# Performance work log

Measured on AMD Instinct MI355X. Metric: run time of the kernel, lower is better.

## Reference

```python
import jax, jax.numpy as jnp
import numpy as np

N_USERS, N_ITEMS, D, B = 16384, 4096, 64, 2048
NAN_FRAC = 0.7
EPS = 1e-8


def setup_inputs() -> dict:
    key = jax.random.key(0)
    k1, k2, k3, k4, k5 = jax.random.split(key, 5)
    ratings = jax.random.uniform(k1, (N_USERS, N_ITEMS), jnp.float32, 1.0, 5.0)
    miss = jax.random.uniform(k2, (N_USERS, N_ITEMS)) < NAN_FRAC
    rating_matrix = jnp.where(miss, jnp.nan, ratings)
    user_embeddings = jax.random.normal(k3, (N_USERS, D), jnp.float32)
    user_indices = jax.random.randint(k4, (B,), 0, N_USERS)
    item_indices = jax.random.randint(k5, (B,), 0, N_ITEMS)
    return {
        "rating_matrix": rating_matrix,
        "user_embeddings": user_embeddings,
        "user_indices": user_indices,
        "item_indices": item_indices,
    }


def reference(rating_matrix, user_embeddings, user_indices, item_indices):
    n_users = rating_matrix.shape[0]

    # per-user average over non-NaN ratings (0.0 if user has no ratings)
    valid_r = ~jnp.isnan(rating_matrix)                      # [N, I]
    r0 = jnp.where(valid_r, rating_matrix, 0.0)
    cnt = valid_r.sum(axis=1)
    avg_ratings = jnp.where(cnt > 0, r0.sum(axis=1) / jnp.maximum(cnt, 1), 0.0)  # [N]

    u = user_embeddings[user_indices]                        # [B, d]
    # cosine similarity of each query user vs all users
    dots = jnp.einsum('bd,nd->bn', u, user_embeddings)       # [B, N]
    mag_u = jnp.linalg.norm(u, axis=1, keepdims=True)        # [B, 1]
    mag_v = jnp.linalg.norm(user_embeddings, axis=1)[None]   # [1, N]
    sim = dots / (mag_u * mag_v + EPS)                       # [B, N]

    # ratings of all users on each query item
    ratings_col = rating_matrix[:, item_indices].T           # [B, N]
    mask = ~jnp.isnan(ratings_col)                           # valid neighbor ratings
    mask = mask & (jnp.arange(n_users)[None, :] != user_indices[:, None])  # exclude self

    diff = jnp.where(mask, ratings_col - avg_ratings[None, :], 0.0)
    sim_m = jnp.where(mask, sim, 0.0)
    num = (diff * sim_m).sum(axis=1)                         # [B]
    den = jnp.abs(sim_m).sum(axis=1)                         # [B]
    den_safe = jnp.where(den == 0, 1.0, den)

    avg_u = avg_ratings[user_indices]
    return jnp.where(den == 0, avg_u, avg_u + num / den_safe)
```

## Files before the change

kernel.cpp:

```cpp
#include <hip/hip_runtime.h>
#include <math.h>

#define NU   16384
#define NI   4096
#define DDIM 64
#define BB   2048

typedef unsigned short u16;
typedef unsigned char  u8;
typedef __attribute__((ext_vector_type(8))) short short8;
typedef __attribute__((ext_vector_type(4))) float f32x4;

static __device__ __forceinline__ u16 f2bf(float f) {
    union { float f; unsigned int u; } v; v.f = f;
    unsigned int u = v.u + 0x7FFFu + ((v.u >> 16) & 1u);
    return (u16)(u >> 16);
}

static __device__ __forceinline__ u8 enc_r(float r) {
    return (u8)__float2uint_rz(fmaf(r, 50.f, -48.5f));
}

__global__ __launch_bounds__(256) void k_qprep(
    const float* __restrict__ E, const int* __restrict__ uidx,
    u16* __restrict__ Ubf, int2* __restrict__ qinfo)
{
    const int lane = threadIdx.x & 63;
    const int b = blockIdx.x * 4 + (threadIdx.x >> 6);
    const int ub = uidx[b];
    const float e = E[(size_t)ub * DDIM + lane];
    float ss = e * e;
#pragma unroll
    for (int o = 32; o > 0; o >>= 1) ss += __shfl_xor(ss, o);
    Ubf[b * DDIM + lane] = f2bf(e);
    if (lane == 0) qinfo[b] = make_int2(ub, __float_as_int(rsqrtf(ss)));
}

__global__ __launch_bounds__(256, 8) void k_stream(
    const float* __restrict__ R, const float* __restrict__ E,
    const int* __restrict__ iidx,
    float2* __restrict__ avgInv, u8* __restrict__ Gq)
{
    __shared__ u16 s_ii[BB];
    __shared__ u8  wrow[4][NI];
    const int tid  = threadIdx.x;
    const int lane = tid & 63;
    const int wid  = tid >> 6;

    for (int t = tid; t < BB; t += 256) s_ii[t] = (u16)iidx[t];
    __syncthreads();

    const int wg = blockIdx.x * 4 + wid;
#pragma unroll 1
    for (int rr = 0; rr < 2; ++rr) {
        const int n = wg * 2 + rr;
        const float4* R4 = (const float4*)(R + (size_t)n * NI);
        const float e = E[(size_t)n * DDIM + lane];

        float sum = 0.f;
        unsigned cnti = 0;
#pragma unroll 1
        for (int h = 0; h < 2; ++h) {
            float4 v[8];
#pragma unroll
            for (int j = 0; j < 8; ++j) v[j] = R4[(h * 8 + j) * 64 + lane];
#pragma unroll
            for (int j = 0; j < 8; ++j) {
                const float4 x = v[j];
                sum += (x.x == x.x ? x.x : 0.f);
                sum += (x.y == x.y ? x.y : 0.f);
                sum += (x.z == x.z ? x.z : 0.f);
                sum += (x.w == x.w ? x.w : 0.f);
                cnti += (unsigned)__popcll(__ballot(x.x == x.x));
                cnti += (unsigned)__popcll(__ballot(x.y == x.y));
                cnti += (unsigned)__popcll(__ballot(x.z == x.z));
                cnti += (unsigned)__popcll(__ballot(x.w == x.w));
                uchar4 q;
                q.x = enc_r(x.x); q.y = enc_r(x.y); q.z = enc_r(x.z); q.w = enc_r(x.w);
                *(uchar4*)&wrow[wid][((h * 8 + j) * 64 + lane) * 4] = q;
            }
        }
        float ss = e * e;
#pragma unroll
        for (int o = 32; o > 0; o >>= 1) {
            ss  += __shfl_xor(ss, o);
            sum += __shfl_xor(sum, o);
        }
        if (lane == 0) {
            const float C = (float)cnti;
            avgInv[n] = make_float2((C > 0.f) ? (sum / C) : 0.f, rsqrtf(ss));
        }
        asm volatile("s_waitcnt lgkmcnt(0)" ::: "memory");

        u8* Gn = Gq + (size_t)n * BB;
#pragma unroll
        for (int t = 0; t < 8; ++t) {
            const int b4 = (t * 64 + lane) * 4;
            const ushort4 ii = *(const ushort4*)&s_ii[b4];
            uchar4 q;
            q.x = wrow[wid][ii.x];
            q.y = wrow[wid][ii.y];
            q.z = wrow[wid][ii.z];
            q.w = wrow[wid][ii.w];
            *(uchar4*)&Gn[b4] = q;
        }
    }
}

__global__ __launch_bounds__(256) void k_accum(
    const float* __restrict__ E, const u16* __restrict__ Ubf,
    const u8* __restrict__ Gq, const float2* __restrict__ avgInv,
    const int2* __restrict__ qinfo, float2* __restrict__ partials)
{
    const int tid  = threadIdx.x;
    const int lane = tid & 63;
    const int wid  = tid >> 6;
    const int lo   = lane & 15;
    const int hi   = lane >> 4;
    const int n0   = blockIdx.x * 16;

    short8 a[2];
#pragma unroll
    for (int kg = 0; kg < 2; ++kg) {
        const float* ep = E + (size_t)(n0 + lo) * DDIM + kg * 32 + hi * 8;
        const float4 e0 = *(const float4*)(ep);
        const float4 e1 = *(const float4*)(ep + 4);
        union { short8 v; u16 u[8]; } t;
        t.u[0] = f2bf(e0.x); t.u[1] = f2bf(e0.y); t.u[2] = f2bf(e0.z); t.u[3] = f2bf(e0.w);
        t.u[4] = f2bf(e1.x); t.u[5] = f2bf(e1.y); t.u[6] = f2bf(e1.z); t.u[7] = f2bf(e1.w);
        a[kg] = t.v;
    }
    float avr[4], ivr[4];
#pragma unroll
    for (int r = 0; r < 4; ++r) {
        const float2 ai = avgInv[n0 + hi * 4 + r];
        avr[r] = ai.x; ivr[r] = ai.y;
    }

    float2* pout = partials + (size_t)blockIdx.x * BB;

#pragma unroll 1
    for (int j = 0; j < 32; ++j) {
        const int b0 = (j * 4 + wid) * 16;
        const int2 q = qinfo[b0 + lo];
        const float inv_mu = __int_as_float(q.y);

        const short8 bf0 = *(const short8*)(Ubf + (size_t)(b0 + lo) * DDIM + hi * 8);
        const short8 bf1 = *(const short8*)(Ubf + (size_t)(b0 + lo) * DDIM + 32 + hi * 8);

        f32x4 c = {0.f, 0.f, 0.f, 0.f};
        c = __builtin_amdgcn_mfma_f32_16x16x32_bf16(a[0], bf0, c, 0, 0, 0);
        c = __builtin_amdgcn_mfma_f32_16x16x32_bf16(a[1], bf1, c, 0, 0, 0);

        float fnum = 0.f, fden = 0.f;
#pragma unroll
        for (int r = 0; r < 4; ++r) {
            const int nr = n0 + hi * 4 + r;
            const u8 qg = Gq[(size_t)nr * BB + b0 + lo];
            const bool valid = (qg != 0) && (nr != q.x);
            const float gv = (float)(int)qg * 0.02f + 0.98f;
            const float s  = valid ? c[r] * (inv_mu * ivr[r]) : 0.f;
            fnum += (gv - avr[r]) * s;
            fden += fabsf(s);
        }
        fnum += __shfl_xor(fnum, 16); fden += __shfl_xor(fden, 16);
        fnum += __shfl_xor(fnum, 32); fden += __shfl_xor(fden, 32);
        if (lane < 16) pout[b0 + lane] = make_float2(fnum, fden);
    }
}

__global__ __launch_bounds__(256) void k_final(
    const float2* __restrict__ partials, const int2* __restrict__ qinfo,
    const float2* __restrict__ avgInv, float* __restrict__ out)
{
    __shared__ float sn[8][32], sd[8][32];
    const int tid = threadIdx.x;
    const int bl  = tid & 31;
    const int ch  = tid >> 5;
    const int b   = blockIdx.x * 32 + bl;
    float n = 0.f, d = 0.f;
    for (int blk = ch; blk < NU / 16; blk += 8) {
        const float2 p = partials[(size_t)blk * BB + b];
        n += p.x; d += p.y;
    }
    sn[ch][bl] = n; sd[ch][bl] = d;
    __syncthreads();
    if (tid < 32) {
        float N = 0.f, D = 0.f;
#pragma unroll
        for (int c2 = 0; c2 < 8; ++c2) { N += sn[c2][tid]; D += sd[c2][tid]; }
        const int bb = blockIdx.x * 32 + tid;
        const float au = avgInv[qinfo[bb].x].x;
        out[bb] = (D == 0.f) ? au : (au + N / D);
    }
}

extern "C" void kernel_launch(void* const* d_in, const int* in_sizes, int n_in,
                              void* d_out, int out_size, void* d_ws, size_t ws_size,
                              hipStream_t stream)
{
    const float* R    = (const float*)d_in[0];
    const float* E    = (const float*)d_in[1];
    const int*   uidx = (const int*)d_in[2];
    const int*   iidx = (const int*)d_in[3];
    float* out = (float*)d_out;

    char* p = (char*)d_ws;
    float2* parts  = (float2*)p;  p += (size_t)(NU / 16) * BB * 8;
    u8*     Gq     = (u8*)p;      p += (size_t)NU * BB;
    u16*    Ubf    = (u16*)p;     p += (size_t)BB * DDIM * 2;
    int2*   qinfo  = (int2*)p;    p += (size_t)BB * 8;
    float2* avgInv = (float2*)p;  p += (size_t)NU * 8;

    k_qprep<<<BB / 4, 256, 0, stream>>>(E, uidx, Ubf, qinfo);
    k_stream<<<NU / 8, 256, 0, stream>>>(R, E, iidx, avgInv, Gq);
    k_accum<<<NU / 16, 256, 0, stream>>>(E, Ubf, Gq, avgInv, qinfo, parts);
    k_final<<<BB / 32, 256, 0, stream>>>(parts, qinfo, avgInv, out);
}
```

Baseline: 444.2 us.

## Software-pipeline rating row loads in k_stream with double-buffered LDS rows

k_stream now unrolls its two rows per wave by hand and issues the global loads for the second rating row while the first row is being processed. This overlaps HBM latency with compute. Each wave gets two LDS row buffers, and the per-row count moves from ballot/popcount to a float counter reduced by shuffles. The cost is a doubled LDS footprint, more registers (launch bounds lowered from 8 to 4 blocks per CU), and therefore lower occupancy.

```diff
diff --git a/kernel.cpp b/kernel.cpp
--- a/kernel.cpp
+++ b/kernel.cpp
@@ -36,13 +36,13 @@
     if (lane == 0) qinfo[b] = make_int2(ub, __float_as_int(rsqrtf(ss)));
 }
 
-__global__ __launch_bounds__(256, 8) void k_stream(
+__global__ __launch_bounds__(256, 4) void k_stream(
     const float* __restrict__ R, const float* __restrict__ E,
     const int* __restrict__ iidx,
     float2* __restrict__ avgInv, u8* __restrict__ Gq)
 {
     __shared__ u16 s_ii[BB];
-    __shared__ u8  wrow[4][NI];
+    __shared__ u8  wrow[4][2][NI];
     const int tid  = threadIdx.x;
     const int lane = tid & 63;
     const int wid  = tid >> 6;
@@ -50,58 +50,110 @@
     for (int t = tid; t < BB; t += 256) s_ii[t] = (u16)iidx[t];
     __syncthreads();
 
-    const int wg = blockIdx.x * 4 + wid;
-#pragma unroll 1
-    for (int rr = 0; rr < 2; ++rr) {
-        const int n = wg * 2 + rr;
-        const float4* R4 = (const float4*)(R + (size_t)n * NI);
-        const float e = E[(size_t)n * DDIM + lane];
-
-        float sum = 0.f;
-        unsigned cnti = 0;
-#pragma unroll 1
-        for (int h = 0; h < 2; ++h) {
-            float4 v[8];
-#pragma unroll
-            for (int j = 0; j < 8; ++j) v[j] = R4[(h * 8 + j) * 64 + lane];
-#pragma unroll
-            for (int j = 0; j < 8; ++j) {
-                const float4 x = v[j];
-                sum += (x.x == x.x ? x.x : 0.f);
-                sum += (x.y == x.y ? x.y : 0.f);
-                sum += (x.z == x.z ? x.z : 0.f);
-                sum += (x.w == x.w ? x.w : 0.f);
-                cnti += (unsigned)__popcll(__ballot(x.x == x.x));
-                cnti += (unsigned)__popcll(__ballot(x.y == x.y));
-                cnti += (unsigned)__popcll(__ballot(x.z == x.z));
-                cnti += (unsigned)__popcll(__ballot(x.w == x.w));
-                uchar4 q;
-                q.x = enc_r(x.x); q.y = enc_r(x.y); q.z = enc_r(x.z); q.w = enc_r(x.w);
-                *(uchar4*)&wrow[wid][((h * 8 + j) * 64 + lane) * 4] = q;
-            }
-        }
-        float ss = e * e;
+    const int n0 = (blockIdx.x * 4 + wid) * 2;
+    const float4* R0 = (const float4*)(R + (size_t)n0 * NI);
+    const float4* R1 = (const float4*)(R + (size_t)(n0 + 1) * NI);
+
+    const float e0 = E[(size_t)n0 * DDIM + lane];
+    const float e1 = E[(size_t)(n0 + 1) * DDIM + lane];
+
+    float4 X[8], Y[8];
+#pragma unroll
+    for (int j = 0; j < 8; ++j) X[j] = R0[j * 64 + lane];
+#pragma unroll
+    for (int j = 0; j < 8; ++j) Y[j] = R0[(8 + j) * 64 + lane];
+
+    float sum0 = 0.f, cnt0 = 0.f, sum1 = 0.f, cnt1 = 0.f;
+
+#pragma unroll
+    for (int j = 0; j < 8; ++j) {
+        const float4 x = X[j];
+        if (x.x == x.x) { sum0 += x.x; cnt0 += 1.f; }
+        if (x.y == x.y) { sum0 += x.y; cnt0 += 1.f; }
+        if (x.z == x.z) { sum0 += x.z; cnt0 += 1.f; }
+        if (x.w == x.w) { sum0 += x.w; cnt0 += 1.f; }
+        uchar4 q;
+        q.x = enc_r(x.x); q.y = enc_r(x.y); q.z = enc_r(x.z); q.w = enc_r(x.w);
+        *(uchar4*)&wrow[wid][0][(j * 64 + lane) * 4] = q;
+        X[j] = R1[j * 64 + lane];
+    }
+#pragma unroll
+    for (int j = 0; j < 8; ++j) {
+        const float4 x = Y[j];
+        if (x.x == x.x) { sum0 += x.x; cnt0 += 1.f; }
+        if (x.y == x.y) { sum0 += x.y; cnt0 += 1.f; }
+        if (x.z == x.z) { sum0 += x.z; cnt0 += 1.f; }
+        if (x.w == x.w) { sum0 += x.w; cnt0 += 1.f; }
+        uchar4 q;
+        q.x = enc_r(x.x); q.y = enc_r(x.y); q.z = enc_r(x.z); q.w = enc_r(x.w);
+        *(uchar4*)&wrow[wid][0][((8 + j) * 64 + lane) * 4] = q;
+        Y[j] = R1[(8 + j) * 64 + lane];
+    }
+    {
+        float ss = e0 * e0, s = sum0, c = cnt0;
 #pragma unroll
         for (int o = 32; o > 0; o >>= 1) {
-            ss  += __shfl_xor(ss, o);
-            sum += __shfl_xor(sum, o);
-        }
-        if (lane == 0) {
-            const float C = (float)cnti;
-            avgInv[n] = make_float2((C > 0.f) ? (sum / C) : 0.f, rsqrtf(ss));
-        }
-        asm volatile("s_waitcnt lgkmcnt(0)" ::: "memory");
-
-        u8* Gn = Gq + (size_t)n * BB;
-#pragma unroll
-        for (int t = 0; t < 8; ++t) {
-            const int b4 = (t * 64 + lane) * 4;
+            ss += __shfl_xor(ss, o); s += __shfl_xor(s, o); c += __shfl_xor(c, o);
+        }
+        if (lane == 0) avgInv[n0] = make_float2((c > 0.f) ? (s / c) : 0.f, rsqrtf(ss));
+    }
+    asm volatile("s_waitcnt lgkmcnt(0)" ::: "memory");
+    {
+        u8* Gn = Gq + (size_t)n0 * BB;
+#pragma unroll
+        for (int t8 = 0; t8 < 8; ++t8) {
+            const int b4 = (t8 * 64 + lane) * 4;
             const ushort4 ii = *(const ushort4*)&s_ii[b4];
             uchar4 q;
-            q.x = wrow[wid][ii.x];
-            q.y = wrow[wid][ii.y];
-            q.z = wrow[wid][ii.z];
-            q.w = wrow[wid][ii.w];
+            q.x = wrow[wid][0][ii.x];
+            q.y = wrow[wid][0][ii.y];
+            q.z = wrow[wid][0][ii.z];
+            q.w = wrow[wid][0][ii.w];
+            *(uchar4*)&Gn[b4] = q;
+        }
+    }
+#pragma unroll
+    for (int j = 0; j < 8; ++j) {
+        const float4 x = X[j];
+        if (x.x == x.x) { sum1 += x.x; cnt1 += 1.f; }
+        if (x.y == x.y) { sum1 += x.y; cnt1 += 1.f; }
+        if (x.z == x.z) { sum1 += x.z; cnt1 += 1.f; }
+        if (x.w == x.w) { sum1 += x.w; cnt1 += 1.f; }
+        uchar4 q;
+        q.x = enc_r(x.x); q.y = enc_r(x.y); q.z = enc_r(x.z); q.w = enc_r(x.w);
+        *(uchar4*)&wrow[wid][1][(j * 64 + lane) * 4] = q;
+    }
+#pragma unroll
+    for (int j = 0; j < 8; ++j) {
+        const float4 x = Y[j];
+        if (x.x == x.x) { sum1 += x.x; cnt1 += 1.f; }
+        if (x.y == x.y) { sum1 += x.y; cnt1 += 1.f; }
+        if (x.z == x.z) { sum1 += x.z; cnt1 += 1.f; }
+        if (x.w == x.w) { sum1 += x.w; cnt1 += 1.f; }
+        uchar4 q;
+        q.x = enc_r(x.x); q.y = enc_r(x.y); q.z = enc_r(x.z); q.w = enc_r(x.w);
+        *(uchar4*)&wrow[wid][1][((8 + j) * 64 + lane) * 4] = q;
+    }
+    {
+        float ss = e1 * e1, s = sum1, c = cnt1;
+#pragma unroll
+        for (int o = 32; o > 0; o >>= 1) {
+            ss += __shfl_xor(ss, o); s += __shfl_xor(s, o); c += __shfl_xor(c, o);
+        }
+        if (lane == 0) avgInv[n0 + 1] = make_float2((c > 0.f) ? (s / c) : 0.f, rsqrtf(ss));
+    }
+    asm volatile("s_waitcnt lgkmcnt(0)" ::: "memory");
+    {
+        u8* Gn = Gq + (size_t)(n0 + 1) * BB;
+#pragma unroll
+        for (int t8 = 0; t8 < 8; ++t8) {
+            const int b4 = (t8 * 64 + lane) * 4;
+            const ushort4 ii = *(const ushort4*)&s_ii[b4];
+            uchar4 q;
+            q.x = wrow[wid][1][ii.x];
+            q.y = wrow[wid][1][ii.y];
+            q.z = wrow[wid][1][ii.z];
+            q.w = wrow[wid][1][ii.w];
             *(uchar4*)&Gn[b4] = q;
         }
     }
```

After: 438.8 us. No clear change (-1.2%).
